# Optimization experiments

Measured on AMD Instinct MI355X. Metric: run time of the kernel, lower is better.

Reference implementation:

```python
import jax, jax.numpy as jnp
import numpy as np

N = 4096
INPUT_DIM = 256
HID = 64        # per-head dim == hidden_dim
HEADS = 4
OUT = 256
AIN = 2 * HID   # hidden + positional concat


def sinusoidal_pe(n, d):
    pos = jnp.arange(n, dtype=jnp.float32)[:, None]
    div = jnp.exp(jnp.arange(0, d, 2, dtype=jnp.float32) * (-np.log(10000.0) / d))
    pe = jnp.zeros((n, d), dtype=jnp.float32)
    pe = pe.at[:, 0::2].set(jnp.sin(pos * div))
    pe = pe.at[:, 1::2].set(jnp.cos(pos * div))
    return pe


def layer_norm(x, g, b, eps=1e-5):
    m = x.mean(-1, keepdims=True)
    v = ((x - m) ** 2).mean(-1, keepdims=True)
    return (x - m) / jnp.sqrt(v + eps) * g + b


def setup_inputs() -> dict:
    key = jax.random.key(0)
    ks = jax.random.split(key, 24)
    s = 0.02
    inp = {
        'Z': jax.random.normal(ks[0], (N, INPUT_DIM), jnp.float32),
        'Z_g': jax.random.normal(ks[1], (N, HID), jnp.float32),
        'Z_c': jax.random.normal(ks[2], (N, HID), jnp.float32),
        'adjacency_matrix': jax.random.randint(ks[3], (N, N), 0, 2).astype(jnp.float32),
        'Wq': s * jax.random.normal(ks[4], (AIN, HID * HEADS), jnp.float32),
        'bq': jnp.zeros((HID * HEADS,), jnp.float32),
        'Wk': s * jax.random.normal(ks[5], (AIN, HID * HEADS), jnp.float32),
        'bk': jnp.zeros((HID * HEADS,), jnp.float32),
        'Wv': s * jax.random.normal(ks[6], (AIN, HID * HEADS), jnp.float32),
        'bv': jnp.zeros((HID * HEADS,), jnp.float32),
        'Wo': s * jax.random.normal(ks[7], (HID * HEADS, OUT), jnp.float32),
        'bo': jnp.zeros((OUT,), jnp.float32),
        'Wr': s * jax.random.normal(ks[8], (INPUT_DIM, OUT), jnp.float32),
        'br': jnp.zeros((OUT,), jnp.float32),
        'ln1_g': jnp.ones((OUT,), jnp.float32),
        'ln1_b': jnp.zeros((OUT,), jnp.float32),
        'ln2_g': jnp.ones((OUT,), jnp.float32),
        'ln2_b': jnp.zeros((OUT,), jnp.float32),
        'f1_w': s * jax.random.normal(ks[9], (OUT, OUT * 4), jnp.float32),
        'f1_b': jnp.zeros((OUT * 4,), jnp.float32),
        'f2_w': s * jax.random.normal(ks[10], (OUT * 4, OUT * 2), jnp.float32),
        'f2_b': jnp.zeros((OUT * 2,), jnp.float32),
        'f3_w': s * jax.random.normal(ks[11], (OUT * 2, OUT), jnp.float32),
        'f3_b': jnp.zeros((OUT,), jnp.float32),
        'structure_weight': jnp.asarray(0.1, jnp.float32),
    }
    return inp


def reference(Z, Z_g, Z_c, adjacency_matrix, Wq, bq, Wk, bk, Wv, bv, Wo, bo,
              Wr, br, ln1_g, ln1_b, ln2_g, ln2_b, f1_w, f1_b, f2_w, f2_b,
              f3_w, f3_b, structure_weight):
    n = Z.shape[0]
    pos = sinusoidal_pe(n, HID)                       # [N, HID]
    Zg_p = jnp.concatenate([Z_g, pos], axis=-1)       # [N, 2*HID]
    Zc_p = jnp.concatenate([Z_c, pos], axis=-1)

    Q = (Zc_p @ Wq + bq).reshape(n, HEADS, HID).transpose(1, 0, 2)  # [H,N,D]
    K = (Zg_p @ Wk + bk).reshape(n, HEADS, HID).transpose(1, 0, 2)
    V = (Zg_p @ Wv + bv).reshape(n, HEADS, HID).transpose(1, 0, 2)

    scores = jnp.einsum('hnd,hmd->hnm', Q, K) / jnp.sqrt(jnp.asarray(HID, jnp.float32))
    structure_mask = (adjacency_matrix == 0).astype(jnp.float32) * -1e9  # [N,N]
    scores = scores + structure_weight * structure_mask[None, :, :]

    attn = jax.nn.softmax(scores, axis=-1)            # [H,N,N]
    attended = jnp.einsum('hnm,hmd->hnd', attn, V)    # [H,N,D]
    attended = attended.transpose(1, 0, 2).reshape(n, HEADS * HID)

    out = attended @ Wo + bo
    residual = Z @ Wr + br
    out = layer_norm(out + residual, ln1_g, ln1_b)

    h = jax.nn.gelu(out @ f1_w + f1_b, approximate=False)
    h = jax.nn.gelu(h @ f2_w + f2_b, approximate=False)
    ffn = h @ f3_w + f3_b
    out = layer_norm(out + ffn, ln2_g, ln2_b)
    return out, attn
```

## Files before the change

kernel.cpp:

```cpp
#include <hip/hip_runtime.h>
#include <cmath>

typedef __attribute__((ext_vector_type(8))) short bf16x8;
typedef __attribute__((ext_vector_type(4))) float f32x4;

#define MFMA16(A,B,C) __builtin_amdgcn_mfma_f32_16x16x32_bf16(A,B,C,0,0,0)

__device__ __forceinline__ ushort f2bf(float x){
  union { float f; unsigned u; } v; v.f = x;
  unsigned r = (v.u + 0x7fffu + ((v.u >> 16) & 1u)) >> 16;
  return (ushort)r;
}
__device__ __forceinline__ float bf2f(ushort h){
  union { unsigned u; float f; } v; v.u = ((unsigned)h) << 16;
  return v.f;
}


__global__ __launch_bounds__(256) void k_cvtZ(const float* Z, ushort* AZ){
  int r = blockIdx.x, c = threadIdx.x;
  AZ[(size_t)r*512 + 256 + c] = f2bf(Z[(size_t)r*256 + c]);
}

__global__ __launch_bounds__(256) void k_transpose(const float* in, ushort* out,
                                                   int K, int N, int RS, int CO){
  __shared__ float t[32][33];
  int kb = blockIdx.x*32, nb = blockIdx.y*32;
  int tx = threadIdx.x & 31, ty = threadIdx.x >> 5;
  for (int i = ty; i < 32; i += 8){
    int k = kb + i, n = nb + tx;
    t[i][tx] = (k < K && n < N) ? in[(size_t)k*N + n] : 0.f;
  }
  __syncthreads();
  for (int i = ty; i < 32; i += 8){
    int n = nb + i, k = kb + tx;
    if (n < N && k < K) out[(size_t)n*RS + CO + k] = f2bf(t[tx][i]);
  }
}

__global__ void k_biasor(const float* bo, const float* br, float* out){
  int j = threadIdx.x;
  out[j] = bo[j] + br[j];
}

__global__ __launch_bounds__(256) void k_adjmask(const float* adj, uint* mask){
  int row = blockIdx.x;
  int wave = threadIdx.x >> 6, lane = threadIdx.x & 63;
  for (int s = 0; s < 16; s++){
    int c = wave*1024 + s*64 + lane;
    float a = adj[(size_t)row*4096 + c];
    unsigned long long b = __ballot(a != 0.f);
    if (lane < 2)
      mask[(size_t)row*128 + wave*32 + s*2 + lane] = (uint)(b >> (lane*32));
  }
}

__global__ __launch_bounds__(256) void k_qkv(
    const float* Zg, const float* Zc,
    const float* Wq, const float* bq, const float* Wk, const float* bk,
    const float* Wv, const float* bv,
    ushort* qb, ushort* kbuf, ushort* vb){
  __shared__ float zcp[16][128], zgp[16][128];
  int r0 = blockIdx.x * 16;
  int t = threadIdx.x;
  for (int i = t; i < 2048; i += 256){
    int row = i >> 7, c = i & 127;
    float vc, vg;
    if (c < 64){
      vc = Zc[(size_t)(r0+row)*64 + c];
      vg = Zg[(size_t)(r0+row)*64 + c];
    } else {
      int ii = (c - 64) >> 1;
      float div = __expf(-0.28782313662425572f * (float)ii);
      float arg = (float)(r0 + row) * div;
      float pe = ((c - 64) & 1) ? cosf(arg) : sinf(arg);
      vc = pe; vg = pe;
    }
    zcp[row][c] = vc; zgp[row][c] = vg;
  }
  __syncthreads();
  float aq[16], ak[16], av[16];
  #pragma unroll
  for (int r = 0; r < 16; r++){ aq[r]=0.f; ak[r]=0.f; av[r]=0.f; }
  int j = t;
  #pragma unroll 4
  for (int k = 0; k < 128; k++){
    float wq = Wq[(size_t)k*256 + j];
    float wk = Wk[(size_t)k*256 + j];
    float wv = Wv[(size_t)k*256 + j];
    #pragma unroll
    for (int r = 0; r < 16; r++){
      float xc = zcp[r][k], xg = zgp[r][k];
      aq[r] = fmaf(xc, wq, aq[r]);
      ak[r] = fmaf(xg, wk, ak[r]);
      av[r] = fmaf(xg, wv, av[r]);
    }
  }
  int h = j >> 6, d = j & 63;
  float bqv = bq[j], bkv = bk[j], bvv = bv[j];
  #pragma unroll
  for (int r = 0; r < 16; r++){
    size_t base = ((size_t)h*4096 + (r0 + r))*64 + d;
    qb[base]   = f2bf((aq[r] + bqv) * 0.125f);
    kbuf[base] = f2bf(ak[r] + bkv);
    vb[base]   = f2bf(av[r] + bvv);
  }
}

__global__ __launch_bounds__(256) void k_vtrans(const ushort* vb, ushort* vtb){
  __shared__ ushort t[64][65];
  int h = blockIdx.y, n0 = blockIdx.x * 64;
  int tx = threadIdx.x & 63, ty = threadIdx.x >> 6;
  for (int i = ty; i < 64; i += 4)
    t[i][tx] = vb[((size_t)h*4096 + n0 + i)*64 + tx];
  __syncthreads();
  for (int i = ty; i < 64; i += 4)
    vtb[((size_t)h*64 + i)*4096 + n0 + tx] = t[tx][i];
}

__global__ __launch_bounds__(1024, 4) void k_attn3(
    const ushort* qb, const ushort* kbuf, const ushort* vtb,
    const uint* maskb, float* attn_out, ushort* az){
  __shared__ __align__(16) char smem[16*4096*2];
  __shared__ float red[16][16];
  __shared__ float rsl[16];
  ushort* pbf = (ushort*)smem;
  float (*pvp)[16][66] = (float(*)[16][66])smem;

  int nb = blockIdx.x;
  int n0 = nb * 16;
  int t = threadIdx.x;
  int wave = t >> 6, lane = t & 63, lr = lane & 15, lg = lane >> 4;

  const uint* mrow = maskb + (size_t)(n0 + lg*4)*128;
  int bp = ((wave & 1) << 4) + lr;

  for (int h = 0; h < 4; h++){
    const ushort* Qh = qb   + ((size_t)h*4096 + n0)*64;
    const ushort* Kh = kbuf + (size_t)h*4096*64;
    const ushort* Vt = vtb  + (size_t)h*64*4096;
    float* aout = attn_out + (size_t)h*4096*4096 + (size_t)n0*4096;

    bf16x8 afr0 = *(const bf16x8*)(Qh + (size_t)lr*64 +  0 + lg*8);
    bf16x8 afr1 = *(const bf16x8*)(Qh + (size_t)lr*64 + 32 + lg*8);

    const ushort* kp0 = Kh + (size_t)(wave*16 + lr)*64 + lg*8;
    float rsum[4] = {0.f, 0.f, 0.f, 0.f};
    #pragma unroll 2
    for (int ct = 0; ct < 16; ct++){
      const ushort* kp = kp0 + (size_t)ct*16384;
      int wi = ct*8 + (wave >> 1);
      bf16x8 b0 = *(const bf16x8*)(kp);
      bf16x8 b1 = *(const bf16x8*)(kp + 32);
      uint m0 = mrow[wi], m1 = mrow[128 + wi], m2 = mrow[256 + wi], m3 = mrow[384 + wi];
      f32x4 acc = {0.f, 0.f, 0.f, 0.f};
      acc = MFMA16(afr0, b0, acc);
      acc = MFMA16(afr1, b1, acc);
      float p0 = ((m0 >> bp) & 1u) ? __expf(acc[0]) : 0.f;
      float p1 = ((m1 >> bp) & 1u) ? __expf(acc[1]) : 0.f;
      float p2 = ((m2 >> bp) & 1u) ? __expf(acc[2]) : 0.f;
      float p3 = ((m3 >> bp) & 1u) ? __expf(acc[3]) : 0.f;
      rsum[0] += p0; rsum[1] += p1; rsum[2] += p2; rsum[3] += p3;
      int col = ct*256 + wave*16 + lr;
      float p4[4] = {p0, p1, p2, p3};
      #pragma unroll
      for (int r = 0; r < 4; r++){
        int row = lg*4 + r;
        pbf[row*4096 + (col ^ ((row & 7) << 3))] = f2bf(p4[r]);
      }
    }
    #pragma unroll
    for (int m = 1; m <= 8; m <<= 1){
      #pragma unroll
      for (int r = 0; r < 4; r++) rsum[r] += __shfl_xor(rsum[r], m, 64);
    }
    if (lr == 0){
      #pragma unroll
      for (int r = 0; r < 4; r++) red[wave][lg*4 + r] = rsum[r];
    }
    __syncthreads();
    if (t < 16){
      float s = 0.f;
      #pragma unroll
      for (int w2 = 0; w2 < 16; w2++) s += red[w2][t];
      rsl[t] = 1.f / s;
    }
    __syncthreads();

    {
      int row = wave;
      float iv = rsl[row];
      int swz = (row & 7) << 3;
      #pragma unroll 2
      for (int q = 0; q < 16; q++){
        int c = q*256 + lane*4;
        const ushort* src = &pbf[row*4096 + (c ^ swz)];
        ushort s4[4];
        *(uint2*)s4 = *(const uint2*)src;
        f32x4 ov = {bf2f(s4[0])*iv, bf2f(s4[1])*iv, bf2f(s4[2])*iv, bf2f(s4[3])*iv};
        __builtin_nontemporal_store(ov, (f32x4*)(aout + (size_t)row*4096 + c));
      }
    }

    f32x4 pacc[4];
    #pragma unroll
    for (int d = 0; d < 4; d++) pacc[d] = (f32x4){0.f,0.f,0.f,0.f};
    #pragma unroll
    for (int ks = 0; ks < 8; ks++){
      int kb2 = wave*256 + ks*32;
      bf16x8 pa = *(const bf16x8*)&pbf[lr*4096 + ((kb2 + lg*8) ^ ((lr & 7) << 3))];
      #pragma unroll
      for (int df = 0; df < 4; df++){
        bf16x8 v8 = *(const bf16x8*)(Vt + (size_t)(df*16 + lr)*4096 + kb2 + lg*8);
        pacc[df] = MFMA16(pa, v8, pacc[df]);
      }
    }

    __syncthreads();
    #pragma unroll
    for (int df = 0; df < 4; df++)
      #pragma unroll
      for (int r = 0; r < 4; r++)
        pvp[wave][lg*4 + r][df*16 + lr] = pacc[df][r];
    __syncthreads();
    {
      int row = t >> 6;
      int d   = t & 63;
      float s = 0.f;
      #pragma unroll
      for (int w2 = 0; w2 < 16; w2++) s += pvp[w2][row][d];
      s *= rsl[row];
      az[(size_t)(n0 + row)*512 + h*64 + d] = f2bf(s);
    }
    __syncthreads();
  }
}

__global__ __launch_bounds__(256) void k_gemm(
    const ushort* A, const ushort* Bt, const float* bias,
    const float* res, float* outf, ushort* outb,
    int M, int N, int K, int mode){
  __shared__ __align__(16) ushort la[64*32];
  __shared__ __align__(16) ushort lb[64*32];
  int mb = blockIdx.x * 64, nb = blockIdx.y * 64;
  int t = threadIdx.x;
  int wave = t >> 6, lane = t & 63, lr = lane & 15, lg = lane >> 4;
  int wm = (wave >> 1) * 32, wn = (wave & 1) * 32;
  f32x4 acc[2][2];
  #pragma unroll
  for (int i = 0; i < 2; i++)
    #pragma unroll
    for (int j = 0; j < 2; j++) acc[i][j] = (f32x4){0.f,0.f,0.f,0.f};

  int srow = t >> 2;
  int scol = 8 * ((t & 3) ^ (srow & 3));
  const ushort* Ag = A  + (size_t)(mb + srow)*K + scol;
  const ushort* Bg = Bt + (size_t)(nb + srow)*K + scol;
  ushort* ldsA = la + (size_t)wave*512;
  ushort* ldsB = lb + (size_t)wave*512;

  for (int k0 = 0; k0 < K; k0 += 32){
    __builtin_amdgcn_global_load_lds((const __attribute__((address_space(1))) unsigned int*)(Ag + k0),
                                     (__attribute__((address_space(3))) unsigned int*)ldsA, 16, 0, 0);
    __builtin_amdgcn_global_load_lds((const __attribute__((address_space(1))) unsigned int*)(Bg + k0),
                                     (__attribute__((address_space(3))) unsigned int*)ldsB, 16, 0, 0);
    __syncthreads();
    #pragma unroll
    for (int i = 0; i < 2; i++){
      int ar = wm + i*16 + lr;
      bf16x8 af = *(const bf16x8*)&la[ar*32 + ((lg ^ (ar & 3)) * 8)];
      #pragma unroll
      for (int j = 0; j < 2; j++){
        int br = wn + j*16 + lr;
        bf16x8 bfg = *(const bf16x8*)&lb[br*32 + ((lg ^ (br & 3)) * 8)];
        acc[i][j] = MFMA16(af, bfg, acc[i][j]);
      }
    }
    __syncthreads();
  }

  #pragma unroll
  for (int i = 0; i < 2; i++)
    #pragma unroll
    for (int j = 0; j < 2; j++){
      int col = nb + wn + j*16 + lr;
      float bv = bias[col];
      #pragma unroll
      for (int r = 0; r < 4; r++){
        int row = mb + wm + i*16 + lg*4 + r;
        float v = acc[i][j][r] + bv;
        if (mode == 0){
          if (res) v += res[(size_t)row*N + col];
          outf[(size_t)row*N + col] = v;
        } else {
          float gl = 0.5f * v * (1.f + erff(v * 0.70710678118f));
          outb[(size_t)row*N + col] = f2bf(gl);
        }
      }
    }
}

__global__ __launch_bounds__(256) void k_ln(const float* X, const float* g, const float* b,
                                            float* outf, ushort* outb){
  int row = blockIdx.x * 4 + (threadIdx.x >> 6);
  int lane = threadIdx.x & 63;
  const float* xr = X + (size_t)row*256;
  f32x4 v = *(const f32x4*)(xr + lane*4);
  float s = v[0] + v[1] + v[2] + v[3];
  #pragma unroll
  for (int m = 32; m >= 1; m >>= 1) s += __shfl_xor(s, m, 64);
  float mean = s * (1.f/256.f);
  float d0[4]; float sq = 0.f;
  #pragma unroll
  for (int e = 0; e < 4; e++){ d0[e] = v[e] - mean; sq += d0[e]*d0[e]; }
  #pragma unroll
  for (int m = 32; m >= 1; m >>= 1) sq += __shfl_xor(sq, m, 64);
  float rstd = rsqrtf(sq * (1.f/256.f) + 1e-5f);
  float o[4];
  #pragma unroll
  for (int e = 0; e < 4; e++)
    o[e] = d0[e]*rstd*g[lane*4 + e] + b[lane*4 + e];
  if (outf){
    f32x4 ov = {o[0], o[1], o[2], o[3]};
    *(f32x4*)(outf + (size_t)row*256 + lane*4) = ov;
  }
  if (outb){
    union { ushort u[4]; uint2 q; } pk;
    #pragma unroll
    for (int e = 0; e < 4; e++) pk.u[e] = f2bf(o[e]);
    *(uint2*)(outb + (size_t)row*256 + lane*4) = pk.q;
  }
}

extern "C" void kernel_launch(void* const* d_in, const int* in_sizes, int n_in,
                              void* d_out, int out_size, void* d_ws, size_t ws_size,
                              hipStream_t stream){
  const float* Z    = (const float*)d_in[0];
  const float* Zg   = (const float*)d_in[1];
  const float* Zc   = (const float*)d_in[2];
  const float* adj  = (const float*)d_in[3];
  const float* Wq   = (const float*)d_in[4];
  const float* bq   = (const float*)d_in[5];
  const float* Wk   = (const float*)d_in[6];
  const float* bk   = (const float*)d_in[7];
  const float* Wv   = (const float*)d_in[8];
  const float* bv   = (const float*)d_in[9];
  const float* Wo   = (const float*)d_in[10];
  const float* bo   = (const float*)d_in[11];
  const float* Wr   = (const float*)d_in[12];
  const float* br   = (const float*)d_in[13];
  const float* ln1g = (const float*)d_in[14];
  const float* ln1b = (const float*)d_in[15];
  const float* ln2g = (const float*)d_in[16];
  const float* ln2b = (const float*)d_in[17];
  const float* f1w  = (const float*)d_in[18];
  const float* f1b  = (const float*)d_in[19];
  const float* f2w  = (const float*)d_in[20];
  const float* f2b  = (const float*)d_in[21];
  const float* f3w  = (const float*)d_in[22];
  const float* f3b  = (const float*)d_in[23];

  float* outF  = (float*)d_out;
  float* attnF = outF + (size_t)4096*256;

  const size_t MB = 1048576;
  char* w = (char*)d_ws;
  ushort* qb    = (ushort*)(w + 0*MB);
  ushort* kbuf  = (ushort*)(w + 2*MB);
  ushort* vtb   = (ushort*)(w + 4*MB);
  ushort* vb    = (ushort*)(w + 6*MB);
  ushort* h1    = (ushort*)(w + 0*MB);
  ushort* AZ    = (ushort*)(w + 8*MB);
  ushort* h2    = (ushort*)(w + 8*MB);
  ushort* BoR   = (ushort*)(w + 12*MB);
  float*  biasOR= (float*)(w + 12*MB + 262144);
  ushort* f1T   = (ushort*)(w + 13*MB);
  ushort* f2T   = (ushort*)(w + 13*MB + 524288);
  ushort* f3T   = (ushort*)(w + 14*MB + 524288);
  float*  X1    = (float*)(w + 15*MB);
  float*  yf    = (float*)(w + 19*MB);
  ushort* yb    = (ushort*)(w + 23*MB);
  uint*   maskb = (uint*)(w + 25*MB);

  k_cvtZ<<<4096, 256, 0, stream>>>(Z, AZ);
  k_adjmask<<<4096, 256, 0, stream>>>(adj, maskb);
  k_transpose<<<dim3(8,  8), 256, 0, stream>>>(Wo,  BoR,  256,  256, 512,   0);
  k_transpose<<<dim3(8,  8), 256, 0, stream>>>(Wr,  BoR,  256,  256, 512, 256);
  k_transpose<<<dim3(8, 32), 256, 0, stream>>>(f1w, f1T,  256, 1024, 256,   0);
  k_transpose<<<dim3(32,16), 256, 0, stream>>>(f2w, f2T, 1024,  512, 1024,  0);
  k_transpose<<<dim3(16, 8), 256, 0, stream>>>(f3w, f3T,  512,  256, 512,   0);
  k_biasor<<<1, 256, 0, stream>>>(bo, br, biasOR);

  k_qkv<<<256, 256, 0, stream>>>(Zg, Zc, Wq, bq, Wk, bk, Wv, bv, qb, kbuf, vb);
  k_vtrans<<<dim3(64, 4), 256, 0, stream>>>(vb, vtb);

  k_attn3<<<256, 1024, 0, stream>>>(qb, kbuf, vtb, maskb, attnF, AZ);

  k_gemm<<<dim3(64, 4), 256, 0, stream>>>(AZ, BoR, biasOR, nullptr, X1, nullptr,
                                          4096, 256, 512, 0);
  k_ln<<<1024, 256, 0, stream>>>(X1, ln1g, ln1b, yf, yb);

  k_gemm<<<dim3(64,16), 256, 0, stream>>>(yb, f1T, f1b, nullptr, nullptr, h1,
                                          4096, 1024, 256, 1);
  k_gemm<<<dim3(64, 8), 256, 0, stream>>>(h1, f2T, f2b, nullptr, nullptr, h2,
                                          4096, 512, 1024, 1);
  k_gemm<<<dim3(64, 4), 256, 0, stream>>>(h2, f3T, f3b, yf, X1, nullptr,
                                          4096, 256, 512, 0);
  k_ln<<<1024, 256, 0, stream>>>(X1, ln2g, ln2b, outF, nullptr);
}
```

Measured before the change: 281.9 us.

## Fuse adjacency bitmask build into attention kernel and restructure attn store loop

Removes the separate k_adjmask kernel. Each attention block now ballots its own 16 adjacency rows into a shared-memory bitmask at kernel start, replacing the global mask reads in the score loop with LDS reads. This drops a kernel launch and the global mask round trip. In exchange, adjacency loading now sits on the attention kernel's critical path instead of overlapping with other work. The normalized-attention write loop is also changed so that each thread covers 4 columns across all 16 rows, instead of each wave writing one row.

New measurement: 284.0 us. No clear change (+0.7%).

```diff
diff --git a/kernel.cpp b/kernel.cpp
--- a/kernel.cpp
+++ b/kernel.cpp
@@ -41,18 +41,6 @@
 __global__ void k_biasor(const float* bo, const float* br, float* out){
   int j = threadIdx.x;
   out[j] = bo[j] + br[j];
-}
-
-__global__ __launch_bounds__(256) void k_adjmask(const float* adj, uint* mask){
-  int row = blockIdx.x;
-  int wave = threadIdx.x >> 6, lane = threadIdx.x & 63;
-  for (int s = 0; s < 16; s++){
-    int c = wave*1024 + s*64 + lane;
-    float a = adj[(size_t)row*4096 + c];
-    unsigned long long b = __ballot(a != 0.f);
-    if (lane < 2)
-      mask[(size_t)row*128 + wave*32 + s*2 + lane] = (uint)(b >> (lane*32));
-  }
 }
 
 __global__ __launch_bounds__(256) void k_qkv(
@@ -120,8 +108,9 @@
 
 __global__ __launch_bounds__(1024, 4) void k_attn3(
     const ushort* qb, const ushort* kbuf, const ushort* vtb,
-    const uint* maskb, float* attn_out, ushort* az){
+    const float* adj, float* attn_out, ushort* az){
   __shared__ __align__(16) char smem[16*4096*2];
+  __shared__ uint  maskL[16][128];
   __shared__ float red[16][16];
   __shared__ float rsl[16];
   ushort* pbf = (ushort*)smem;
@@ -132,7 +121,16 @@
   int t = threadIdx.x;
   int wave = t >> 6, lane = t & 63, lr = lane & 15, lg = lane >> 4;
 
-  const uint* mrow = maskb + (size_t)(n0 + lg*4)*128;
+  {
+    const float* arow = adj + (size_t)(n0 + wave)*4096;
+    for (int s = 0; s < 64; s++){
+      float a = arow[s*64 + lane];
+      unsigned long long b = __ballot(a != 0.f);
+      if (lane < 2) maskL[wave][s*2 + lane] = (uint)(b >> (lane*32));
+    }
+  }
+  __syncthreads();
+
   int bp = ((wave & 1) << 4) + lr;
 
   for (int h = 0; h < 4; h++){
@@ -152,7 +150,10 @@
       int wi = ct*8 + (wave >> 1);
       bf16x8 b0 = *(const bf16x8*)(kp);
       bf16x8 b1 = *(const bf16x8*)(kp + 32);
-      uint m0 = mrow[wi], m1 = mrow[128 + wi], m2 = mrow[256 + wi], m3 = mrow[384 + wi];
+      uint m0 = maskL[lg*4 + 0][wi];
+      uint m1 = maskL[lg*4 + 1][wi];
+      uint m2 = maskL[lg*4 + 2][wi];
+      uint m3 = maskL[lg*4 + 3][wi];
       f32x4 acc = {0.f, 0.f, 0.f, 0.f};
       acc = MFMA16(afr0, b0, acc);
       acc = MFMA16(afr1, b1, acc);
@@ -188,17 +189,15 @@
     __syncthreads();
 
     {
-      int row = wave;
-      float iv = rsl[row];
-      int swz = (row & 7) << 3;
-      #pragma unroll 2
-      for (int q = 0; q < 16; q++){
-        int c = q*256 + lane*4;
-        const ushort* src = &pbf[row*4096 + (c ^ swz)];
+      int c = t * 4;
+      #pragma unroll
+      for (int r = 0; r < 16; r++){
+        float iv = rsl[r];
+        const ushort* src = &pbf[r*4096 + (c ^ ((r & 7) << 3))];
         ushort s4[4];
         *(uint2*)s4 = *(const uint2*)src;
         f32x4 ov = {bf2f(s4[0])*iv, bf2f(s4[1])*iv, bf2f(s4[2])*iv, bf2f(s4[3])*iv};
-        __builtin_nontemporal_store(ov, (f32x4*)(aout + (size_t)row*4096 + c));
+        __builtin_nontemporal_store(ov, (f32x4*)(aout + (size_t)r*4096 + c));
       }
     }
 
@@ -380,10 +379,8 @@
   float*  X1    = (float*)(w + 15*MB);
   float*  yf    = (float*)(w + 19*MB);
   ushort* yb    = (ushort*)(w + 23*MB);
-  uint*   maskb = (uint*)(w + 25*MB);
 
   k_cvtZ<<<4096, 256, 0, stream>>>(Z, AZ);
-  k_adjmask<<<4096, 256, 0, stream>>>(adj, maskb);
   k_transpose<<<dim3(8,  8), 256, 0, stream>>>(Wo,  BoR,  256,  256, 512,   0);
   k_transpose<<<dim3(8,  8), 256, 0, stream>>>(Wr,  BoR,  256,  256, 512, 256);
   k_transpose<<<dim3(8, 32), 256, 0, stream>>>(f1w, f1T,  256, 1024, 256,   0);
@@ -394,7 +391,7 @@
   k_qkv<<<256, 256, 0, stream>>>(Zg, Zc, Wq, bq, Wk, bk, Wv, bv, qb, kbuf, vb);
   k_vtrans<<<dim3(64, 4), 256, 0, stream>>>(vb, vtb);
 
-  k_attn3<<<256, 1024, 0, stream>>>(qb, kbuf, vtb, maskb, attnF, AZ);
+  k_attn3<<<256, 1024, 0, stream>>>(qb, kbuf, vtb, adj, attnF, AZ);
 
   k_gemm<<<dim3(64, 4), 256, 0, stream>>>(AZ, BoR, biasOR, nullptr, X1, nullptr,
                                           4096, 256, 512, 0);
```
